# Performance work log

Hardware: AMD Instinct MI355X
Metric: run time of the kernel (lower is better)

Reference implementation:

```python
import jax, jax.numpy as jnp
import numpy as np

SIZE = 5   # local window side
HEADS = 1

def patch_extract(x, size):
    # x: [B, C, H, W] -> [B, C, size*size, H, W], replicate padding,
    # window index l = i*size + j (row-major over kernel), matching F.unfold.
    p = size // 2
    xp = jnp.pad(x, ((0, 0), (0, 0), (p, p), (p, p)), mode='edge')
    H, W = x.shape[2], x.shape[3]
    windows = [xp[:, :, i:i + H, j:j + W] for i in range(size) for j in range(size)]
    return jnp.stack(windows, axis=2)

def setup_inputs() -> dict:
    key = jax.random.key(0)
    k1, k2, k3, k4 = jax.random.split(key, 4)
    B, C, H, W = 4, 128, 64, 128
    attn = jax.random.normal(k1, (B, HEADS, H * W, SIZE * SIZE), dtype=jnp.float32)
    fmap = jax.random.normal(k2, (B, C, H, W), dtype=jnp.float32)
    Wv = jax.random.normal(k3, (C, C), dtype=jnp.float32) * (1.0 / np.sqrt(C))
    gamma = jax.random.normal(k4, (1,), dtype=jnp.float32)
    return {"attn": attn, "fmap": fmap, "Wv": Wv, "gamma": gamma}

def reference(attn, fmap, Wv, gamma):
    B, C, H, W = fmap.shape
    d = C // HEADS
    L = SIZE * SIZE
    # to_v: 1x1 conv, no bias
    v = jnp.einsum('oc,bchw->bohw', Wv, fmap)
    # local window gather: [B, C, L, H, W]
    v = patch_extract(v, SIZE)
    # 'b (h d) l x y -> b h (x y) d l'
    v = v.reshape(B, HEADS, d, L, H, W)
    v = v.transpose(0, 1, 4, 5, 2, 3).reshape(B, HEADS, H * W, d, L)
    # weighted sum over the local window
    out = jnp.einsum('bhnl,bhndl->bhnd', attn, v)
    # 'b h (x y) d -> b (h d) x y'
    out = out.reshape(B, HEADS, H, W, d).transpose(0, 1, 4, 2, 3).reshape(B, C, H, W)
    return fmap + gamma[0] * out
```

## Files before the change

kernel.cpp:

```cpp
#include <hip/hip_runtime.h>


namespace {
constexpr int Bn = 4, Cn = 128, Hn = 64, Wn = 128, Ln = 25;
constexpr int HWn = Hn * Wn;

constexpr int TY = 4, TX = 16;
constexpr int HY = 8, HX = 24;
constexpr int RS = 136;
constexpr int SVS = 136;
constexpr int WVS = 136;
constexpr int NT = 512;

typedef __attribute__((ext_vector_type(8))) short short8;
typedef __attribute__((ext_vector_type(4))) float f32x4;

__device__ inline unsigned short f2bf(float f) {
    unsigned u = __float_as_uint(f);
    return (unsigned short)((u + 0x7fffu + ((u >> 16) & 1u)) >> 16);
}

__global__ __launch_bounds__(NT, 4) void lsa_fused(
    const float* __restrict__ attn, const float* __restrict__ fmap,
    const float* __restrict__ Wv, const float* __restrict__ gamma,
    float* __restrict__ out)
{
    __shared__ alignas(16) unsigned short hs[HY * HX * RS];
    __shared__ alignas(16) unsigned short sv[TY * TX * SVS];
    __shared__ alignas(16) float at_s[TY * TX * Ln];

    const int tid = threadIdx.x;

    const unsigned bid = blockIdx.x;
    const unsigned logical = (bid & 7u) * 64u + (bid >> 3);
    const int bx  = logical & 7;
    const int byz = logical >> 3;
    const int by  = byz & 15;
    const int b   = byz >> 4;
    const int x0 = bx * TX;
    const int y0 = by * TY;

    float4 va[6], vb[6];
#pragma unroll
    for (int t = 0; t < 6; ++t) {
        const int i = tid + t * NT;
        const int k = i % 6;
        const int r = i / 6;
        const int cp = r & 63;
        const int dy = r >> 6;
        const int ry = min(max(y0 + dy - 2, 0), Hn - 1);
        const int gxb = x0 - 4 + 4 * k;
        const size_t rowb = ((size_t)(b * Cn + 2 * cp)) * HWn + (size_t)ry * Wn;
        if (gxb < 0) {
            const float s0 = fmap[rowb], s1 = fmap[rowb + HWn];
            va[t].x = va[t].y = va[t].z = va[t].w = s0;
            vb[t].x = vb[t].y = vb[t].z = vb[t].w = s1;
        } else if (gxb > Wn - 4) {
            const float s0 = fmap[rowb + Wn - 1], s1 = fmap[rowb + HWn + Wn - 1];
            va[t].x = va[t].y = va[t].z = va[t].w = s0;
            vb[t].x = vb[t].y = vb[t].z = vb[t].w = s1;
        } else {
            va[t] = *(const float4*)&fmap[rowb + gxb];
            vb[t] = *(const float4*)&fmap[rowb + HWn + gxb];
        }
    }
    float4 at_r;
    const int yi_a = tid / 100, j4 = tid - yi_a * 100;
    if (tid < 400) {
        const size_t ab = ((size_t)b * HWn + (size_t)y0 * Wn + x0) * Ln;
        at_r = *(const float4*)&attn[ab + (size_t)yi_a * (Wn * Ln) + j4 * 4];
    }

#pragma unroll
    for (int t = 0; t < 6; ++t) {
        const int i = tid + t * NT;
        const int k = i % 6;
        const int r = i / 6;
        const int cp = r & 63;
        const int dy = r >> 6;
        unsigned short* hbase = &hs[(dy * HX + 4 * k) * RS + 2 * cp];
        *(unsigned*)&hbase[0 * RS] = (unsigned)f2bf(va[t].x) | ((unsigned)f2bf(vb[t].x) << 16);
        *(unsigned*)&hbase[1 * RS] = (unsigned)f2bf(va[t].y) | ((unsigned)f2bf(vb[t].y) << 16);
        *(unsigned*)&hbase[2 * RS] = (unsigned)f2bf(va[t].z) | ((unsigned)f2bf(vb[t].z) << 16);
        *(unsigned*)&hbase[3 * RS] = (unsigned)f2bf(va[t].w) | ((unsigned)f2bf(vb[t].w) << 16);
    }
    if (tid < 400) *(float4*)&at_s[tid * 4] = at_r;
    __syncthreads();

    const int xi = tid & 15, kq = (tid >> 4) & 7, yi = tid >> 7;
    const int p = yi * 16 + xi;
    float acc[16];
#pragma unroll
    for (int j = 0; j < 16; ++j) acc[j] = 0.f;

#pragma unroll
    for (int l = 0; l < Ln; ++l) {
        const int dy = l / 5, dx = l % 5;
        const float a = at_s[p * Ln + l];
        const unsigned short* row = &hs[((yi + dy) * HX + (2 + xi + dx)) * RS + kq * 16];
#pragma unroll
        for (int q = 0; q < 2; ++q) {
            uint4 u = *(const uint4*)&row[q * 8];
            const unsigned w[4] = {u.x, u.y, u.z, u.w};
#pragma unroll
            for (int e = 0; e < 4; ++e) {
                acc[q * 8 + 2 * e + 0] += a * __uint_as_float(w[e] << 16);
                acc[q * 8 + 2 * e + 1] += a * __uint_as_float(w[e] & 0xffff0000u);
            }
        }
    }
    float4 wq[8];
#pragma unroll
    for (int t = 0; t < 8; ++t)
        wq[t] = *(const float4*)&Wv[(size_t)(tid + t * NT) * 4];

    {
        unsigned short* dst = &sv[p * SVS + kq * 16];
#pragma unroll
        for (int q = 0; q < 2; ++q) {
            unsigned pk[4];
#pragma unroll
            for (int e = 0; e < 4; ++e)
                pk[e] = (unsigned)f2bf(acc[q * 8 + 2 * e]) |
                        ((unsigned)f2bf(acc[q * 8 + 2 * e + 1]) << 16);
            uint4 v; v.x = pk[0]; v.y = pk[1]; v.z = pk[2]; v.w = pk[3];
            *(uint4*)&dst[q * 8] = v;
        }
    }
    __syncthreads();

#pragma unroll
    for (int t = 0; t < 8; ++t) {
        const int i4 = tid + t * NT;
        const int r = i4 >> 5;
        const int c = (i4 & 31) * 4;
        uint2 v;
        v.x = (unsigned)f2bf(wq[t].x) | ((unsigned)f2bf(wq[t].y) << 16);
        v.y = (unsigned)f2bf(wq[t].z) | ((unsigned)f2bf(wq[t].w) << 16);
        *(uint2*)&hs[r * WVS + c] = v;
    }
    __syncthreads();

    const int wave = tid >> 6, lane = tid & 63;
    const int m16 = lane & 15, q = lane >> 4;
    const int wrow = wave >> 1;
    const int mhalf = wave & 1;
    const int n = (y0 + wrow) * Wn + x0 + m16;
    const float g = gamma[0];

    short8 bfrag[4];
    {
        const unsigned short* srow = &sv[(wrow * 16 + m16) * SVS + q * 8];
#pragma unroll
        for (int kk = 0; kk < 4; ++kk) bfrag[kk] = *(const short8*)(srow + kk * 32);
    }
    f32x4 accv[4];
#pragma unroll
    for (int t = 0; t < 4; ++t) { f32x4 z = {0.f, 0.f, 0.f, 0.f}; accv[t] = z; }

#pragma unroll
    for (int t = 0; t < 4; ++t) {
        const int mg = mhalf * 4 + t;
        const unsigned short* arow = &hs[(mg * 16 + m16) * WVS + q * 8];
#pragma unroll
        for (int kk = 0; kk < 4; ++kk) {
            short8 af = *(const short8*)(arow + kk * 32);
            accv[t] = __builtin_amdgcn_mfma_f32_16x16x32_bf16(af, bfrag[kk], accv[t], 0, 0, 0);
        }
    }

#pragma unroll
    for (int t = 0; t < 4; ++t) {
        const int mg = mhalf * 4 + t;
#pragma unroll
        for (int r = 0; r < 4; ++r) {
            const int c = mg * 16 + q * 4 + r;
            const size_t idx = ((size_t)(b * Cn + c)) * HWn + n;
            out[idx] = fmap[idx] + g * accv[t][r];
        }
    }
}
}

extern "C" void kernel_launch(void* const* d_in, const int* in_sizes, int n_in,
                              void* d_out, int out_size, void* d_ws, size_t ws_size,
                              hipStream_t stream) {
    const float* attn  = (const float*)d_in[0];
    const float* fmap  = (const float*)d_in[1];
    const float* Wv    = (const float*)d_in[2];
    const float* gamma = (const float*)d_in[3];
    float* out = (float*)d_out;

    lsa_fused<<<dim3(512), NT, 0, stream>>>(attn, fmap, Wv, gamma, out);
}
```

Before: 90.20 us.

## Process two row-tiles per block with ring-buffered halo and prefetch

Each block now covers 8 output rows in two 4-row passes, reusing the overlapping halo rows through an 8-row ring buffer in LDS. Only the 4 new rows are loaded for the second pass, and that load is issued before the first pass's compute. Wv and attention are staged once per block, and the grid is halved. This reduces redundant halo and weight loads but halves block count and raises LDS use, which may reduce occupancy and latency hiding.

```diff
diff --git a/kernel.cpp b/kernel.cpp
--- a/kernel.cpp
+++ b/kernel.cpp
@@ -5,8 +5,8 @@
 constexpr int Bn = 4, Cn = 128, Hn = 64, Wn = 128, Ln = 25;
 constexpr int HWn = Hn * Wn;
 
-constexpr int TY = 4, TX = 16;
-constexpr int HY = 8, HX = 24;
+constexpr int TX = 16;
+constexpr int HX = 24;
 constexpr int RS = 136;
 constexpr int SVS = 136;
 constexpr int WVS = 136;
@@ -20,25 +20,25 @@
     return (unsigned short)((u + 0x7fffu + ((u >> 16) & 1u)) >> 16);
 }
 
-__global__ __launch_bounds__(NT, 4) void lsa_fused(
+__global__ __launch_bounds__(NT, 2) void lsa_fused(
     const float* __restrict__ attn, const float* __restrict__ fmap,
     const float* __restrict__ Wv, const float* __restrict__ gamma,
     float* __restrict__ out)
 {
-    __shared__ alignas(16) unsigned short hs[HY * HX * RS];
-    __shared__ alignas(16) unsigned short sv[TY * TX * SVS];
-    __shared__ alignas(16) float at_s[TY * TX * Ln];
+    __shared__ alignas(16) unsigned short hs[8 * HX * RS];
+    __shared__ alignas(16) unsigned short sv[64 * SVS];
+    __shared__ alignas(16) unsigned short wvs[128 * WVS];
+    __shared__ alignas(16) float at_s[2 * 64 * Ln];
 
     const int tid = threadIdx.x;
 
     const unsigned bid = blockIdx.x;
-    const unsigned logical = (bid & 7u) * 64u + (bid >> 3);
+    const unsigned logical = (bid & 7u) * 32u + (bid >> 3);
     const int bx  = logical & 7;
-    const int byz = logical >> 3;
-    const int by  = byz & 15;
-    const int b   = byz >> 4;
+    const int byb = (logical >> 3) & 7;
+    const int b   = logical >> 6;
     const int x0 = bx * TX;
-    const int y0 = by * TY;
+    const int y0 = byb * 8;
 
     float4 va[6], vb[6];
 #pragma unroll
@@ -64,11 +64,19 @@
             vb[t] = *(const float4*)&fmap[rowb + HWn + gxb];
         }
     }
-    float4 at_r;
-    const int yi_a = tid / 100, j4 = tid - yi_a * 100;
-    if (tid < 400) {
-        const size_t ab = ((size_t)b * HWn + (size_t)y0 * Wn + x0) * Ln;
-        at_r = *(const float4*)&attn[ab + (size_t)yi_a * (Wn * Ln) + j4 * 4];
+    const size_t ab = ((size_t)b * HWn + (size_t)y0 * Wn + x0) * Ln;
+    float4 at0, at1;
+    {
+        const int i4 = tid;
+        const int h = i4 / 400, rem = i4 - h * 400;
+        const int yia = rem / 100, j4 = (rem - yia * 100) * 4;
+        at0 = *(const float4*)&attn[ab + (size_t)h * 12800 + (size_t)yia * 3200 + j4];
+    }
+    if (tid < 288) {
+        const int i4 = tid + 512;
+        const int h = i4 / 400, rem = i4 - h * 400;
+        const int yia = rem / 100, j4 = (rem - yia * 100) * 4;
+        at1 = *(const float4*)&attn[ab + (size_t)h * 12800 + (size_t)yia * 3200 + j4];
     }
 
 #pragma unroll
@@ -84,8 +92,39 @@
         *(unsigned*)&hbase[2 * RS] = (unsigned)f2bf(va[t].z) | ((unsigned)f2bf(vb[t].z) << 16);
         *(unsigned*)&hbase[3 * RS] = (unsigned)f2bf(va[t].w) | ((unsigned)f2bf(vb[t].w) << 16);
     }
-    if (tid < 400) *(float4*)&at_s[tid * 4] = at_r;
-    __syncthreads();
+    *(float4*)&at_s[tid * 4] = at0;
+    if (tid < 288) *(float4*)&at_s[(tid + 512) * 4] = at1;
+    __syncthreads();
+
+    float4 wq[8];
+#pragma unroll
+    for (int t = 0; t < 8; ++t)
+        wq[t] = *(const float4*)&Wv[(size_t)(tid + t * NT) * 4];
+
+    float4 va2[3], vb2[3];
+#pragma unroll
+    for (int t = 0; t < 3; ++t) {
+        const int j = tid + t * NT;
+        const int k = j % 6;
+        const int r = j / 6;
+        const int cp = r & 63;
+        const int dyp = r >> 6;
+        const int ry = min(y0 + 6 + dyp, Hn - 1);
+        const int gxb = x0 - 4 + 4 * k;
+        const size_t rowb = ((size_t)(b * Cn + 2 * cp)) * HWn + (size_t)ry * Wn;
+        if (gxb < 0) {
+            const float s0 = fmap[rowb], s1 = fmap[rowb + HWn];
+            va2[t].x = va2[t].y = va2[t].z = va2[t].w = s0;
+            vb2[t].x = vb2[t].y = vb2[t].z = vb2[t].w = s1;
+        } else if (gxb > Wn - 4) {
+            const float s0 = fmap[rowb + Wn - 1], s1 = fmap[rowb + HWn + Wn - 1];
+            va2[t].x = va2[t].y = va2[t].z = va2[t].w = s0;
+            vb2[t].x = vb2[t].y = vb2[t].z = vb2[t].w = s1;
+        } else {
+            va2[t] = *(const float4*)&fmap[rowb + gxb];
+            vb2[t] = *(const float4*)&fmap[rowb + HWn + gxb];
+        }
+    }
 
     const int xi = tid & 15, kq = (tid >> 4) & 7, yi = tid >> 7;
     const int p = yi * 16 + xi;
@@ -109,11 +148,6 @@
             }
         }
     }
-    float4 wq[8];
-#pragma unroll
-    for (int t = 0; t < 8; ++t)
-        wq[t] = *(const float4*)&Wv[(size_t)(tid + t * NT) * 4];
-
     {
         unsigned short* dst = &sv[p * SVS + kq * 16];
 #pragma unroll
@@ -129,6 +163,19 @@
     }
     __syncthreads();
 
+#pragma unroll
+    for (int t = 0; t < 3; ++t) {
+        const int j = tid + t * NT;
+        const int k = j % 6;
+        const int r = j / 6;
+        const int cp = r & 63;
+        const int dyp = r >> 6;
+        unsigned short* hbase = &hs[(dyp * HX + 4 * k) * RS + 2 * cp];
+        *(unsigned*)&hbase[0 * RS] = (unsigned)f2bf(va2[t].x) | ((unsigned)f2bf(vb2[t].x) << 16);
+        *(unsigned*)&hbase[1 * RS] = (unsigned)f2bf(va2[t].y) | ((unsigned)f2bf(vb2[t].y) << 16);
+        *(unsigned*)&hbase[2 * RS] = (unsigned)f2bf(va2[t].z) | ((unsigned)f2bf(vb2[t].z) << 16);
+        *(unsigned*)&hbase[3 * RS] = (unsigned)f2bf(va2[t].w) | ((unsigned)f2bf(vb2[t].w) << 16);
+    }
 #pragma unroll
     for (int t = 0; t < 8; ++t) {
         const int i4 = tid + t * NT;
@@ -137,7 +184,7 @@
         uint2 v;
         v.x = (unsigned)f2bf(wq[t].x) | ((unsigned)f2bf(wq[t].y) << 16);
         v.y = (unsigned)f2bf(wq[t].z) | ((unsigned)f2bf(wq[t].w) << 16);
-        *(uint2*)&hs[r * WVS + c] = v;
+        *(uint2*)&wvs[r * WVS + c] = v;
     }
     __syncthreads();
 
@@ -145,38 +192,102 @@
     const int m16 = lane & 15, q = lane >> 4;
     const int wrow = wave >> 1;
     const int mhalf = wave & 1;
-    const int n = (y0 + wrow) * Wn + x0 + m16;
     const float g = gamma[0];
 
-    short8 bfrag[4];
-    {
+    {
+        const int n = (y0 + wrow) * Wn + x0 + m16;
+        short8 bfrag[4];
         const unsigned short* srow = &sv[(wrow * 16 + m16) * SVS + q * 8];
 #pragma unroll
         for (int kk = 0; kk < 4; ++kk) bfrag[kk] = *(const short8*)(srow + kk * 32);
-    }
-    f32x4 accv[4];
-#pragma unroll
-    for (int t = 0; t < 4; ++t) { f32x4 z = {0.f, 0.f, 0.f, 0.f}; accv[t] = z; }
-
-#pragma unroll
-    for (int t = 0; t < 4; ++t) {
-        const int mg = mhalf * 4 + t;
-        const unsigned short* arow = &hs[(mg * 16 + m16) * WVS + q * 8];
-#pragma unroll
-        for (int kk = 0; kk < 4; ++kk) {
-            short8 af = *(const short8*)(arow + kk * 32);
-            accv[t] = __builtin_amdgcn_mfma_f32_16x16x32_bf16(af, bfrag[kk], accv[t], 0, 0, 0);
-        }
-    }
-
-#pragma unroll
-    for (int t = 0; t < 4; ++t) {
-        const int mg = mhalf * 4 + t;
-#pragma unroll
-        for (int r = 0; r < 4; ++r) {
-            const int c = mg * 16 + q * 4 + r;
-            const size_t idx = ((size_t)(b * Cn + c)) * HWn + n;
-            out[idx] = fmap[idx] + g * accv[t][r];
+        f32x4 accv[4];
+#pragma unroll
+        for (int t = 0; t < 4; ++t) { f32x4 z = {0.f, 0.f, 0.f, 0.f}; accv[t] = z; }
+#pragma unroll
+        for (int t = 0; t < 4; ++t) {
+            const int mg = mhalf * 4 + t;
+            const unsigned short* arow = &wvs[(mg * 16 + m16) * WVS + q * 8];
+#pragma unroll
+            for (int kk = 0; kk < 4; ++kk) {
+                short8 af = *(const short8*)(arow + kk * 32);
+                accv[t] = __builtin_amdgcn_mfma_f32_16x16x32_bf16(af, bfrag[kk], accv[t], 0, 0, 0);
+            }
+        }
+#pragma unroll
+        for (int t = 0; t < 4; ++t) {
+            const int mg = mhalf * 4 + t;
+#pragma unroll
+            for (int r = 0; r < 4; ++r) {
+                const int c = mg * 16 + q * 4 + r;
+                const size_t idx = ((size_t)(b * Cn + c)) * HWn + n;
+                out[idx] = fmap[idx] + g * accv[t][r];
+            }
+        }
+    }
+
+#pragma unroll
+    for (int j = 0; j < 16; ++j) acc[j] = 0.f;
+#pragma unroll
+    for (int l = 0; l < Ln; ++l) {
+        const int dy = l / 5, dx = l % 5;
+        const float a = at_s[1600 + p * Ln + l];
+        const unsigned short* row = &hs[((((4 + yi + dy) & 7)) * HX + (2 + xi + dx)) * RS + kq * 16];
+#pragma unroll
+        for (int q2 = 0; q2 < 2; ++q2) {
+            uint4 u = *(const uint4*)&row[q2 * 8];
+            const unsigned w[4] = {u.x, u.y, u.z, u.w};
+#pragma unroll
+            for (int e = 0; e < 4; ++e) {
+                acc[q2 * 8 + 2 * e + 0] += a * __uint_as_float(w[e] << 16);
+                acc[q2 * 8 + 2 * e + 1] += a * __uint_as_float(w[e] & 0xffff0000u);
+            }
+        }
+    }
+    __syncthreads();
+
+    {
+        unsigned short* dst = &sv[p * SVS + kq * 16];
+#pragma unroll
+        for (int q2 = 0; q2 < 2; ++q2) {
+            unsigned pk[4];
+#pragma unroll
+            for (int e = 0; e < 4; ++e)
+                pk[e] = (unsigned)f2bf(acc[q2 * 8 + 2 * e]) |
+                        ((unsigned)f2bf(acc[q2 * 8 + 2 * e + 1]) << 16);
+            uint4 v; v.x = pk[0]; v.y = pk[1]; v.z = pk[2]; v.w = pk[3];
+            *(uint4*)&dst[q2 * 8] = v;
+        }
+    }
+    __syncthreads();
+
+    {
+        const int n = (y0 + 4 + wrow) * Wn + x0 + m16;
+        short8 bfrag[4];
+        const unsigned short* srow = &sv[(wrow * 16 + m16) * SVS + q * 8];
+#pragma unroll
+        for (int kk = 0; kk < 4; ++kk) bfrag[kk] = *(const short8*)(srow + kk * 32);
+        f32x4 accv[4];
+#pragma unroll
+        for (int t = 0; t < 4; ++t) { f32x4 z = {0.f, 0.f, 0.f, 0.f}; accv[t] = z; }
+#pragma unroll
+        for (int t = 0; t < 4; ++t) {
+            const int mg = mhalf * 4 + t;
+            const unsigned short* arow = &wvs[(mg * 16 + m16) * WVS + q * 8];
+#pragma unroll
+            for (int kk = 0; kk < 4; ++kk) {
+                short8 af = *(const short8*)(arow + kk * 32);
+                accv[t] = __builtin_amdgcn_mfma_f32_16x16x32_bf16(af, bfrag[kk], accv[t], 0, 0, 0);
+            }
+        }
+#pragma unroll
+        for (int t = 0; t < 4; ++t) {
+            const int mg = mhalf * 4 + t;
+#pragma unroll
+            for (int r = 0; r < 4; ++r) {
+                const int c = mg * 16 + q * 4 + r;
+                const size_t idx = ((size_t)(b * Cn + c)) * HWn + n;
+                out[idx] = fmap[idx] + g * accv[t][r];
+            }
         }
     }
 }
@@ -191,5 +302,5 @@
     const float* gamma = (const float*)d_in[3];
     float* out = (float*)d_out;
 
-    lsa_fused<<<dim3(512), NT, 0, stream>>>(attn, fmap, Wv, gamma, out);
+    lsa_fused<<<dim3(256), NT, 0, stream>>>(attn, fmap, Wv, gamma, out);
 }
```

Result: no change. 90.75 us (+0.6%).

## Compute local window weighted sum as sparse-banded fp16 MFMA matmul

Applied to the files above, without the earlier changes.

Replaces the scalar 25-tap weighted sum over the halo with a matrix multiply. The halo tile is stored channel-major in fp16, and the attention weights are scattered into a zero-filled banded matrix of 64 pixels by 192 halo positions, so MFMA f16 instructions compute the window aggregation. This moves the ALU and LDS-read heavy inner loop onto matrix cores at the price of roughly 8x redundant multiply-by-zero work, extra zero-fill and scatter passes with an added barrier, and fp16 rounding of both fmap and attention values. Shared memory is also re-partitioned so the two buffers are reused for the later Wv projection.

```diff
diff --git a/kernel.cpp b/kernel.cpp
--- a/kernel.cpp
+++ b/kernel.cpp
@@ -5,19 +5,26 @@
 constexpr int Bn = 4, Cn = 128, Hn = 64, Wn = 128, Ln = 25;
 constexpr int HWn = Hn * Wn;
 
-constexpr int TY = 4, TX = 16;
-constexpr int HY = 8, HX = 24;
-constexpr int RS = 136;
+constexpr int TX = 16, TY = 4;
+constexpr int RTS = 200;
+constexpr int MS  = 200;
 constexpr int SVS = 136;
 constexpr int WVS = 136;
-constexpr int NT = 512;
+constexpr int NT  = 512;
 
 typedef __attribute__((ext_vector_type(8))) short short8;
+typedef _Float16 half8 __attribute__((ext_vector_type(8)));
 typedef __attribute__((ext_vector_type(4))) float f32x4;
 
 __device__ inline unsigned short f2bf(float f) {
     unsigned u = __float_as_uint(f);
     return (unsigned short)((u + 0x7fffu + ((u >> 16) & 1u)) >> 16);
+}
+__device__ inline unsigned short f2h(float f) {
+    union { _Float16 h; unsigned short u; } c; c.h = (_Float16)f; return c.u;
+}
+__device__ inline unsigned pk2h(float a, float b) {
+    return (unsigned)f2h(a) | ((unsigned)f2h(b) << 16);
 }
 
 __global__ __launch_bounds__(NT, 4) void lsa_fused(
@@ -25,9 +32,9 @@
     const float* __restrict__ Wv, const float* __restrict__ gamma,
     float* __restrict__ out)
 {
-    __shared__ alignas(16) unsigned short hs[HY * HX * RS];
-    __shared__ alignas(16) unsigned short sv[TY * TX * SVS];
-    __shared__ alignas(16) float at_s[TY * TX * Ln];
+    __shared__ alignas(16) unsigned short smem[38400];
+    unsigned short* const Rt = smem;
+    unsigned short* const Mb = smem + 25600;
 
     const int tid = threadIdx.x;
 
@@ -44,12 +51,12 @@
 #pragma unroll
     for (int t = 0; t < 6; ++t) {
         const int i = tid + t * NT;
-        const int k = i % 6;
+        const int k6 = i % 6;
         const int r = i / 6;
         const int cp = r & 63;
-        const int dy = r >> 6;
-        const int ry = min(max(y0 + dy - 2, 0), Hn - 1);
-        const int gxb = x0 - 4 + 4 * k;
+        const int s = r >> 6;
+        const int ry = min(max(y0 + s - 2, 0), Hn - 1);
+        const int gxb = x0 - 4 + 4 * k6;
         const size_t rowb = ((size_t)(b * Cn + 2 * cp)) * HWn + (size_t)ry * Wn;
         if (gxb < 0) {
             const float s0 = fmap[rowb], s1 = fmap[rowb + HWn];
@@ -64,93 +71,100 @@
             vb[t] = *(const float4*)&fmap[rowb + HWn + gxb];
         }
     }
+    const size_t ab = ((size_t)b * HWn + (size_t)y0 * Wn + x0) * Ln;
     float4 at_r;
-    const int yi_a = tid / 100, j4 = tid - yi_a * 100;
-    if (tid < 400) {
-        const size_t ab = ((size_t)b * HWn + (size_t)y0 * Wn + x0) * Ln;
-        at_r = *(const float4*)&attn[ab + (size_t)yi_a * (Wn * Ln) + j4 * 4];
-    }
+    const int yia = tid / 100, j4 = tid - yia * 100;
+    if (tid < 400)
+        at_r = *(const float4*)&attn[ab + (size_t)yia * (Wn * Ln) + (size_t)j4 * 4];
 
 #pragma unroll
     for (int t = 0; t < 6; ++t) {
         const int i = tid + t * NT;
-        const int k = i % 6;
+        const int k6 = i % 6;
         const int r = i / 6;
         const int cp = r & 63;
-        const int dy = r >> 6;
-        unsigned short* hbase = &hs[(dy * HX + 4 * k) * RS + 2 * cp];
-        *(unsigned*)&hbase[0 * RS] = (unsigned)f2bf(va[t].x) | ((unsigned)f2bf(vb[t].x) << 16);
-        *(unsigned*)&hbase[1 * RS] = (unsigned)f2bf(va[t].y) | ((unsigned)f2bf(vb[t].y) << 16);
-        *(unsigned*)&hbase[2 * RS] = (unsigned)f2bf(va[t].z) | ((unsigned)f2bf(vb[t].z) << 16);
-        *(unsigned*)&hbase[3 * RS] = (unsigned)f2bf(va[t].w) | ((unsigned)f2bf(vb[t].w) << 16);
-    }
-    if (tid < 400) *(float4*)&at_s[tid * 4] = at_r;
-    __syncthreads();
-
-    const int xi = tid & 15, kq = (tid >> 4) & 7, yi = tid >> 7;
-    const int p = yi * 16 + xi;
-    float acc[16];
-#pragma unroll
-    for (int j = 0; j < 16; ++j) acc[j] = 0.f;
-
-#pragma unroll
-    for (int l = 0; l < Ln; ++l) {
-        const int dy = l / 5, dx = l % 5;
-        const float a = at_s[p * Ln + l];
-        const unsigned short* row = &hs[((yi + dy) * HX + (2 + xi + dx)) * RS + kq * 16];
-#pragma unroll
-        for (int q = 0; q < 2; ++q) {
-            uint4 u = *(const uint4*)&row[q * 8];
-            const unsigned w[4] = {u.x, u.y, u.z, u.w};
-#pragma unroll
-            for (int e = 0; e < 4; ++e) {
-                acc[q * 8 + 2 * e + 0] += a * __uint_as_float(w[e] << 16);
-                acc[q * 8 + 2 * e + 1] += a * __uint_as_float(w[e] & 0xffff0000u);
-            }
-        }
-    }
+        const int s = r >> 6;
+        unsigned short* d0 = &Rt[(2 * cp) * RTS + s * 24 + 4 * k6];
+        uint2 wa; wa.x = pk2h(va[t].x, va[t].y); wa.y = pk2h(va[t].z, va[t].w);
+        uint2 wb; wb.x = pk2h(vb[t].x, vb[t].y); wb.y = pk2h(vb[t].z, vb[t].w);
+        *(uint2*)d0 = wa;
+        *(uint2*)(d0 + RTS) = wb;
+    }
+    {
+        const uint4 z4 = {0u, 0u, 0u, 0u};
+        for (int i = tid; i < 1600; i += NT)
+            *(uint4*)&Mb[i * 8] = z4;
+    }
+    __syncthreads();
+
+    if (tid < 400) {
+        const float ae[4] = {at_r.x, at_r.y, at_r.z, at_r.w};
+#pragma unroll
+        for (int e = 0; e < 4; ++e) {
+            const int t2 = j4 * 4 + e;
+            const int xi2 = t2 / 25, l = t2 - 25 * xi2;
+            const int dy = l / 5, dx = l - 5 * dy;
+            Mb[(yia * 16 + xi2) * MS + (yia + dy) * 24 + 2 + xi2 + dx] = f2h(ae[e]);
+        }
+    }
+    __syncthreads();
+
     float4 wq[8];
 #pragma unroll
     for (int t = 0; t < 8; ++t)
         wq[t] = *(const float4*)&Wv[(size_t)(tid + t * NT) * 4];
 
+    const int wave = tid >> 6, lane = tid & 63;
+    const int m16 = lane & 15, q = lane >> 4;
+    const int row = wave >> 1;
+    const int chalf = wave & 1;
+
+    f32x4 acv[4];
+#pragma unroll
+    for (int t = 0; t < 4; ++t) { f32x4 z = {0.f, 0.f, 0.f, 0.f}; acv[t] = z; }
+
+#pragma unroll
+    for (int kk = 0; kk < 6; ++kk) {
+        half8 bfr = *(const half8*)&Mb[(row * 16 + m16) * MS + q * 8 + kk * 32];
+#pragma unroll
+        for (int ct = 0; ct < 4; ++ct) {
+            half8 af = *(const half8*)&Rt[(chalf * 64 + ct * 16 + m16) * RTS + q * 8 + kk * 32];
+            acv[ct] = __builtin_amdgcn_mfma_f32_16x16x32_f16(af, bfr, acv[ct], 0, 0, 0);
+        }
+    }
+    __syncthreads();
+
+    unsigned short* const sv  = Mb;
+    unsigned short* const wvs = Rt;
     {
-        unsigned short* dst = &sv[p * SVS + kq * 16];
-#pragma unroll
-        for (int q = 0; q < 2; ++q) {
-            unsigned pk[4];
-#pragma unroll
-            for (int e = 0; e < 4; ++e)
-                pk[e] = (unsigned)f2bf(acc[q * 8 + 2 * e]) |
-                        ((unsigned)f2bf(acc[q * 8 + 2 * e + 1]) << 16);
-            uint4 v; v.x = pk[0]; v.y = pk[1]; v.z = pk[2]; v.w = pk[3];
-            *(uint4*)&dst[q * 8] = v;
-        }
-    }
-    __syncthreads();
-
+        const int px = row * 16 + m16;
+#pragma unroll
+        for (int ct = 0; ct < 4; ++ct) {
+            const int c0 = chalf * 64 + ct * 16 + q * 4;
+            uint2 w;
+            w.x = (unsigned)f2bf(acv[ct][0]) | ((unsigned)f2bf(acv[ct][1]) << 16);
+            w.y = (unsigned)f2bf(acv[ct][2]) | ((unsigned)f2bf(acv[ct][3]) << 16);
+            *(uint2*)&sv[px * SVS + c0] = w;
+        }
+    }
 #pragma unroll
     for (int t = 0; t < 8; ++t) {
         const int i4 = tid + t * NT;
-        const int r = i4 >> 5;
-        const int c = (i4 & 31) * 4;
+        const int rr = i4 >> 5;
+        const int cc = (i4 & 31) * 4;
         uint2 v;
         v.x = (unsigned)f2bf(wq[t].x) | ((unsigned)f2bf(wq[t].y) << 16);
         v.y = (unsigned)f2bf(wq[t].z) | ((unsigned)f2bf(wq[t].w) << 16);
-        *(uint2*)&hs[r * WVS + c] = v;
-    }
-    __syncthreads();
-
-    const int wave = tid >> 6, lane = tid & 63;
-    const int m16 = lane & 15, q = lane >> 4;
-    const int wrow = wave >> 1;
-    const int mhalf = wave & 1;
-    const int n = (y0 + wrow) * Wn + x0 + m16;
+        *(uint2*)&wvs[rr * WVS + cc] = v;
+    }
+    __syncthreads();
+
+    const int n = (y0 + row) * Wn + x0 + m16;
     const float g = gamma[0];
 
     short8 bfrag[4];
     {
-        const unsigned short* srow = &sv[(wrow * 16 + m16) * SVS + q * 8];
+        const unsigned short* srow = &sv[(row * 16 + m16) * SVS + q * 8];
 #pragma unroll
         for (int kk = 0; kk < 4; ++kk) bfrag[kk] = *(const short8*)(srow + kk * 32);
     }
@@ -160,18 +174,17 @@
 
 #pragma unroll
     for (int t = 0; t < 4; ++t) {
-        const int mg = mhalf * 4 + t;
-        const unsigned short* arow = &hs[(mg * 16 + m16) * WVS + q * 8];
+        const int mg = chalf * 4 + t;
+        const unsigned short* arow = &wvs[(mg * 16 + m16) * WVS + q * 8];
 #pragma unroll
         for (int kk = 0; kk < 4; ++kk) {
             short8 af = *(const short8*)(arow + kk * 32);
             accv[t] = __builtin_amdgcn_mfma_f32_16x16x32_bf16(af, bfrag[kk], accv[t], 0, 0, 0);
         }
     }
-
 #pragma unroll
     for (int t = 0; t < 4; ++t) {
-        const int mg = mhalf * 4 + t;
+        const int mg = chalf * 4 + t;
 #pragma unroll
         for (int r = 0; r < 4; ++r) {
             const int c = mg * 16 + q * 4 + r;
```

Result: faster. 86.94 us (-3.6%).
